# Optimization experiments

Measured on AMD Instinct MI355X. Metric: run time of the kernel, lower is better.

The kernel has to match this reference:

```python
import jax, jax.numpy as jnp
import numpy as np


def setup_inputs() -> dict:
    key = jax.random.key(0)
    k1, k2, k3 = jax.random.split(key, 3)
    B, F, D = 1024, 784, 512
    x = jax.random.normal(k1, (B, F), dtype=jnp.float32)
    # keras 'uniform' initializer ~ U(-0.05, 0.05)
    Wmin = jax.random.uniform(k2, (D, F), dtype=jnp.float32, minval=-0.05, maxval=0.05)
    Wmax = jax.random.uniform(k3, (D, F), dtype=jnp.float32, minval=-0.05, maxval=0.05)
    return {"x": x, "Wmin": Wmin, "Wmax": Wmax}


def reference(x, Wmin, Wmax):
    # x: [B, F]; Wmin, Wmax: [D, F]
    # L1[b,d] = min_f (x[b,f] - Wmin[d,f]); L2[b,d] = min_f (Wmax[d,f] - x[b,f])
    L1 = jnp.min(x[:, None, :] - Wmin[None, :, :], axis=2)  # [B, D]
    L2 = jnp.min(Wmax[None, :, :] - x[:, None, :], axis=2)  # [B, D]
    # activation is None (linear) in this config
    return jnp.minimum(L1, L2)  # [B, D]
```

## Files before the change

### kernel.cpp

```cpp
#include <hip/hip_runtime.h>


constexpr int F_DIM = 784;
constexpr int BM = 128;
constexpr int BN = 32;
constexpr int ZSPLIT = 14;
constexpr int FS = F_DIM / ZSPLIT;
constexpr int LSTR = 60;
constexpr int NF4 = FS / 4;

typedef float f4v __attribute__((ext_vector_type(4)));
typedef float f2v __attribute__((ext_vector_type(2)));

__global__ __launch_bounds__(256, 4)
void dendral_init_kernel(float* __restrict__ out) {
  const int i = blockIdx.x * 256 + threadIdx.x;
  const float inf = __builtin_inff();
  f4v v = {inf, inf, inf, inf};
  ((f4v*)out)[i] = v;
}

__device__ inline void atomic_min_float(float* addr, float v) {
  if (v >= 0.0f) atomicMin((int*)addr, __float_as_int(v));
  else           atomicMax((unsigned int*)addr, __float_as_uint(v));
}

__device__ __forceinline__ void cell_min(float& acc, const f4v xv,
                                         const f4v nv, const f4v wv) {
  const f2v xlo = xv.xy, xhi = xv.zw;
  const f2v nlo = nv.xy, nhi = nv.zw;
  const f2v wlo = wv.xy, whi = wv.zw;
  f2v d0, d1, e0, e1;
  asm("v_pk_add_f32 %0, %1, %2 neg_lo:[0,1] neg_hi:[0,1]"
      : "=v"(d0) : "v"(xlo), "v"(nlo));
  asm("v_pk_add_f32 %0, %1, %2 neg_lo:[0,1] neg_hi:[0,1]"
      : "=v"(d1) : "v"(xhi), "v"(nhi));
  asm("v_pk_add_f32 %0, %1, %2 neg_lo:[0,1] neg_hi:[0,1]"
      : "=v"(e0) : "v"(wlo), "v"(xlo));
  asm("v_pk_add_f32 %0, %1, %2 neg_lo:[0,1] neg_hi:[0,1]"
      : "=v"(e1) : "v"(whi), "v"(xhi));
  float m0, m1, m2;
  asm("v_min3_f32 %0, %1, %2, %3"
      : "=v"(m0) : "v"(d0.x), "v"(d0.y), "v"(d1.x));
  asm("v_min3_f32 %0, %1, %2, %3"
      : "=v"(m1) : "v"(d1.y), "v"(e0.x), "v"(e0.y));
  asm("v_min3_f32 %0, %1, %2, %3"
      : "=v"(m2) : "v"(e1.x), "v"(e1.y), "v"(m0));
  asm("v_min3_f32 %0, %1, %2, %3"
      : "=v"(acc) : "v"(m1), "v"(m2), "v"(acc));
}

__global__ __launch_bounds__(256, 2)
void dendral_min_kernel(const float* __restrict__ x,
                        const float* __restrict__ wmin,
                        const float* __restrict__ wmax,
                        float* __restrict__ out, int D) {
  __shared__ float lwn[BN * LSTR];
  __shared__ float lwx[BN * LSTR];

  const int t  = threadIdx.x;
  const int tx = t & 15;
  const int ty = t >> 4;
  const int b0 = blockIdx.x * BM;
  const int d0 = blockIdx.y * BN;
  const int f0 = blockIdx.z * FS;

#pragma unroll
  for (int k = 0; k < 4; ++k) {
    const int i = t + 256 * k;
    if (i < 64 * NF4) {
      const int row = i / NF4;
      const int c4  = i % NF4;
      const int wr  = row & 31;
      const float* src = (row < 32 ? wmin : wmax)
                         + (size_t)(d0 + wr) * F_DIM + f0 + c4 * 4;
      float* dst = (row < 32 ? lwn : lwx) + wr * LSTR + c4 * 4;
      *(f4v*)dst = *(const f4v*)src;
    }
  }
  __syncthreads();

  const size_t xoff = (size_t)(b0 + ty) * F_DIM + f0;

  float acc[8][2];
#pragma unroll
  for (int r = 0; r < 8; ++r)
#pragma unroll
    for (int c = 0; c < 2; ++c)
      acc[r][c] = __builtin_inff();

  const float* lnb0 = &lwn[tx * LSTR];
  const float* lnb1 = &lwn[(tx + 16) * LSTR];
  const float* lwb0 = &lwx[tx * LSTR];
  const float* lwb1 = &lwx[(tx + 16) * LSTR];

#pragma unroll 2
  for (int fi = 0; fi < NF4; ++fi) {
    f4v xv[8];
#pragma unroll
    for (int r = 0; r < 8; ++r)
      xv[r] = *(const f4v*)(x + xoff + (size_t)r * 16 * F_DIM + fi * 4);
    f4v nv0 = *(const f4v*)(lnb0 + fi * 4);
    f4v nv1 = *(const f4v*)(lnb1 + fi * 4);
    f4v wv0 = *(const f4v*)(lwb0 + fi * 4);
    f4v wv1 = *(const f4v*)(lwb1 + fi * 4);
#pragma unroll
    for (int r = 0; r < 8; ++r) {
      cell_min(acc[r][0], xv[r], nv0, wv0);
      cell_min(acc[r][1], xv[r], nv1, wv1);
    }
  }

#pragma unroll
  for (int r = 0; r < 8; ++r)
#pragma unroll
    for (int c = 0; c < 2; ++c) {
      const int b = b0 + ty + 16 * r;
      const int d = d0 + tx + 16 * c;
      atomic_min_float(&out[(size_t)b * D + d], acc[r][c]);
    }
}

extern "C" void kernel_launch(void* const* d_in, const int* in_sizes, int n_in,
                              void* d_out, int out_size, void* d_ws, size_t ws_size,
                              hipStream_t stream) {
  const float* x    = (const float*)d_in[0];
  const float* wmin = (const float*)d_in[1];
  const float* wmax = (const float*)d_in[2];
  float* out = (float*)d_out;
  const int B = in_sizes[0] / F_DIM;
  const int D = in_sizes[1] / F_DIM;

  dendral_init_kernel<<<(B * D) / 1024, 256, 0, stream>>>(out);

  dim3 grid(B / BM, D / BN, ZSPLIT);
  dendral_min_kernel<<<grid, 256, 0, stream>>>(x, wmin, wmax, out, D);
  (void)n_in; (void)d_ws; (void)ws_size; (void)out_size;
}
```

Baseline: 100.1 us.

## Replace atomic split-F reduction with workspace partials plus separate reduce kernel

Each F-split block now writes its partial minima to a per-split slice of the workspace with plain stores, and a second kernel reduces the fourteen slices into the output. This removes the init kernel and the global atomic min/max traffic. In exchange it writes and rereads about fourteen times the output size through memory. The old atomic path is kept as a fallback when the workspace is too small.

```diff
diff --git a/kernel.cpp b/kernel.cpp
--- a/kernel.cpp
+++ b/kernel.cpp
@@ -50,11 +50,12 @@
       : "=v"(acc) : "v"(m1), "v"(m2), "v"(acc));
 }
 
-__global__ __launch_bounds__(256, 2)
-void dendral_min_kernel(const float* __restrict__ x,
-                        const float* __restrict__ wmin,
-                        const float* __restrict__ wmax,
-                        float* __restrict__ out, int D) {
+template <bool USE_WS>
+__device__ __forceinline__ void dendral_body(const float* __restrict__ x,
+                                             const float* __restrict__ wmin,
+                                             const float* __restrict__ wmax,
+                                             float* __restrict__ dst,
+                                             int D) {
   __shared__ float lwn[BN * LSTR];
   __shared__ float lwx[BN * LSTR];
 
@@ -74,8 +75,8 @@
       const int wr  = row & 31;
       const float* src = (row < 32 ? wmin : wmax)
                          + (size_t)(d0 + wr) * F_DIM + f0 + c4 * 4;
-      float* dst = (row < 32 ? lwn : lwx) + wr * LSTR + c4 * 4;
-      *(f4v*)dst = *(const f4v*)src;
+      float* d_ = (row < 32 ? lwn : lwx) + wr * LSTR + c4 * 4;
+      *(f4v*)d_ = *(const f4v*)src;
     }
   }
   __syncthreads();
@@ -117,8 +118,46 @@
     for (int c = 0; c < 2; ++c) {
       const int b = b0 + ty + 16 * r;
       const int d = d0 + tx + 16 * c;
-      atomic_min_float(&out[(size_t)b * D + d], acc[r][c]);
+      if (USE_WS)
+        dst[(size_t)b * D + d] = acc[r][c];
+      else
+        atomic_min_float(&dst[(size_t)b * D + d], acc[r][c]);
     }
+}
+
+__global__ __launch_bounds__(256, 2)
+void dendral_part_kernel(const float* __restrict__ x,
+                         const float* __restrict__ wmin,
+                         const float* __restrict__ wmax,
+                         float* __restrict__ ws, int D, int BD) {
+  float* dst = ws + (size_t)blockIdx.z * BD;
+  dendral_body<true>(x, wmin, wmax, dst, D);
+}
+
+__global__ __launch_bounds__(256, 2)
+void dendral_min_kernel(const float* __restrict__ x,
+                        const float* __restrict__ wmin,
+                        const float* __restrict__ wmax,
+                        float* __restrict__ out, int D) {
+  dendral_body<false>(x, wmin, wmax, out, D);
+}
+
+__global__ __launch_bounds__(256, 2)
+void dendral_reduce_kernel(const float* __restrict__ ws,
+                           float* __restrict__ out, int BD) {
+  const int i4 = blockIdx.x * 256 + threadIdx.x;
+  const f4v* w = (const f4v*)ws;
+  const int n4 = BD >> 2;
+  f4v m = w[i4];
+#pragma unroll
+  for (int z = 1; z < ZSPLIT; ++z) {
+    f4v v = w[(size_t)z * n4 + i4];
+    m.x = fminf(m.x, v.x);
+    m.y = fminf(m.y, v.y);
+    m.z = fminf(m.z, v.z);
+    m.w = fminf(m.w, v.w);
+  }
+  ((f4v*)out)[i4] = m;
 }
 
 extern "C" void kernel_launch(void* const* d_in, const int* in_sizes, int n_in,
@@ -130,10 +169,19 @@
   float* out = (float*)d_out;
   const int B = in_sizes[0] / F_DIM;
   const int D = in_sizes[1] / F_DIM;
-
-  dendral_init_kernel<<<(B * D) / 1024, 256, 0, stream>>>(out);
+  const int BD = B * D;
+  const size_t need = (size_t)BD * ZSPLIT * sizeof(float);
 
   dim3 grid(B / BM, D / BN, ZSPLIT);
-  dendral_min_kernel<<<grid, 256, 0, stream>>>(x, wmin, wmax, out, D);
-  (void)n_in; (void)d_ws; (void)ws_size; (void)out_size;
+
+  if (d_ws != nullptr && ws_size >= need) {
+    dendral_part_kernel<<<grid, 256, 0, stream>>>(x, wmin, wmax,
+                                                  (float*)d_ws, D, BD);
+    dendral_reduce_kernel<<<BD / 1024, 256, 0, stream>>>((const float*)d_ws,
+                                                         out, BD);
+  } else {
+    dendral_init_kernel<<<BD / 1024, 256, 0, stream>>>(out);
+    dendral_min_kernel<<<grid, 256, 0, stream>>>(x, wmin, wmax, out, D);
+  }
+  (void)n_in; (void)out_size;
 }
```

Result: no change. 98.18 us (-1.9%).
